# Kernel tuning notes

Hardware: AMD Instinct MI355X
Metric: run time of the kernel (lower is better)

## Reference

```python
import jax, jax.numpy as jnp
import numpy as np

NEG_SLOPE = 0.01  # torch F.leaky_relu default


def setup_inputs() -> dict:
    key = jax.random.key(0)
    k1, k2, k3, k4 = jax.random.split(key, 4)
    B, N, F_in, F_out = 16, 2048, 128, 128
    stdv = 1.0 / np.sqrt(F_out)
    h = jax.random.normal(k1, (B, N, F_in), dtype=jnp.float32)
    adj = jax.random.uniform(k2, (B, N, N), dtype=jnp.float32)
    W = jax.random.uniform(k3, (F_in, F_out), minval=-stdv, maxval=stdv, dtype=jnp.float32)
    a = jax.random.uniform(k4, (2 * F_out, 1), minval=-stdv, maxval=stdv, dtype=jnp.float32)
    return {"h": h, "adj": adj, "W": W, "a": a}


def reference(h, adj, W, a):
    # Wh: [B, N, F_out]
    Wh = jnp.matmul(h, W)
    F_out = W.shape[1]
    a1 = a[:F_out, 0]  # [F_out]
    a2 = a[F_out:, 0]  # [F_out]
    # concat-score factorizes: e[b,i,j] = leaky(Wh[b,i]@a1 + Wh[b,j]@a2)
    f1 = jnp.einsum('bnf,f->bn', Wh, a1)  # [B, N]
    f2 = jnp.einsum('bnf,f->bn', Wh, a2)  # [B, N]
    e = jax.nn.leaky_relu(f1[:, :, None] + f2[:, None, :], negative_slope=NEG_SLOPE)  # [B,N,N]
    # NOTE: original softmax is over dim=1 (row index i), faithfully preserved
    attention = jax.nn.softmax(e, axis=1)
    h_prime = jnp.einsum('bij,bjf->bif', attention, Wh)  # bmm
    return h_prime
```

## Files before the change

### kernel.cpp

```cpp
#include <hip/hip_runtime.h>

#define BB 16
#define NN 2048
#define FF 128
#define NEG 0.01f
#define CH 32
#define CL (NN / CH)

__global__ __launch_bounds__(256) void k_wh(const float* __restrict__ h,
                                            const float* __restrict__ Wg,
                                            const float* __restrict__ a,
                                            float* __restrict__ Wh,
                                            float* __restrict__ f1,
                                            float* __restrict__ f2) {
    __shared__ float Ws[64 * 128];
    __shared__ float hsT[64 * 36];

    const int tid  = threadIdx.x;
    const int fg   = tid & 31;
    const int slot = tid >> 5;
    const int f4   = fg * 4;
    const int rowBase = blockIdx.x * 32;

    float acc[4][4];
#pragma unroll
    for (int r = 0; r < 4; ++r)
#pragma unroll
        for (int c = 0; c < 4; ++c) acc[r][c] = 0.f;

    const float4* Wg4 = (const float4*)Wg;
    const float4* hg4 = (const float4*)h;

    for (int kh = 0; kh < 128; kh += 64) {
        __syncthreads();
        for (int idx = tid; idx < 64 * 32; idx += 256) {
            int kk = idx >> 5, ff = idx & 31;
            ((float4*)Ws)[kk * 32 + ff] = Wg4[(size_t)(kh + kk) * 32 + ff];
        }
#pragma unroll
        for (int pass = 0; pass < 2; ++pass) {
            int idx = pass * 256 + tid;
            int kq = idx & 15, row = idx >> 4;
            float4 h4 = hg4[(size_t)(rowBase + row) * 32 + (kh >> 2) + kq];
            hsT[(kq * 4 + 0) * 36 + row] = h4.x;
            hsT[(kq * 4 + 1) * 36 + row] = h4.y;
            hsT[(kq * 4 + 2) * 36 + row] = h4.z;
            hsT[(kq * 4 + 3) * 36 + row] = h4.w;
        }
        __syncthreads();
#pragma unroll 8
        for (int kk = 0; kk < 64; ++kk) {
            float4 wv = *(const float4*)&Ws[kk * 128 + f4];
            float4 hv = *(const float4*)&hsT[kk * 36 + slot * 4];
            acc[0][0] += hv.x * wv.x; acc[0][1] += hv.x * wv.y; acc[0][2] += hv.x * wv.z; acc[0][3] += hv.x * wv.w;
            acc[1][0] += hv.y * wv.x; acc[1][1] += hv.y * wv.y; acc[1][2] += hv.y * wv.z; acc[1][3] += hv.y * wv.w;
            acc[2][0] += hv.z * wv.x; acc[2][1] += hv.z * wv.y; acc[2][2] += hv.z * wv.z; acc[2][3] += hv.z * wv.w;
            acc[3][0] += hv.w * wv.x; acc[3][1] += hv.w * wv.y; acc[3][2] += hv.w * wv.z; acc[3][3] += hv.w * wv.w;
        }
    }

    const float4* ag4 = (const float4*)a;
    float4 a1v = ag4[fg];
    float4 a2v = ag4[32 + fg];

#pragma unroll
    for (int r = 0; r < 4; ++r) {
        int row = rowBase + slot * 4 + r;
        float4 o; o.x = acc[r][0]; o.y = acc[r][1]; o.z = acc[r][2]; o.w = acc[r][3];
        *(float4*)&Wh[(size_t)row * 128 + f4] = o;
        float p1 = acc[r][0] * a1v.x + acc[r][1] * a1v.y + acc[r][2] * a1v.z + acc[r][3] * a1v.w;
        float p2 = acc[r][0] * a2v.x + acc[r][1] * a2v.y + acc[r][2] * a2v.z + acc[r][3] * a2v.w;
#pragma unroll
        for (int m = 16; m >= 1; m >>= 1) {
            p1 += __shfl_xor(p1, m);
            p2 += __shfl_xor(p2, m);
        }
        if (fg == 0) { f1[row] = p1; f2[row] = p2; }
    }
}

__device__ __forceinline__ float wave_incl_scan(float s, int lane) {
#pragma unroll
    for (int m = 1; m <= 32; m <<= 1) {
        float o = __shfl_up(s, m);
        if (lane >= m) s += o;
    }
    return s;
}

#define WAVE_SYNC() do { __builtin_amdgcn_wave_barrier(); asm volatile("" ::: "memory"); } while (0)

__global__ __launch_bounds__(1024) void k_sort2(const float* __restrict__ f1,
                                                const float* __restrict__ f2,
                                                float* __restrict__ SF1g,
                                                float* __restrict__ PAg,
                                                float* __restrict__ SAg,
                                                float* __restrict__ SKg,
                                                int* __restrict__ PERM,
                                                int* __restrict__ KIDX) {
    __shared__ float sKey[NN];
    __shared__ int   sIdx[NN];
    __shared__ float wtot[16];

    const int tid  = threadIdx.x;
    const int lane = tid & 63;
    const int w    = tid >> 6;
    const int b    = blockIdx.x & 15;
    const int task = blockIdx.x >> 4;

    const float* f1b = f1 + b * NN;
    const float* f2b = f2 + b * NN;

    if (task == 0) {
        for (int i = tid; i < NN; i += 1024) sKey[i] = f1b[i];
    } else {
        for (int i = tid; i < NN; i += 1024) { sKey[i] = f2b[i]; sIdx[i] = i; }
    }

    int prevj = 1024;
    for (int k = 2; k <= NN; k <<= 1) {
        for (int j = k >> 1; j > 0; j >>= 1) {
            if (j >= 128 || prevj >= 128) __syncthreads();
            else WAVE_SYNC();
            int mask = j - 1;
            int i   = ((tid & ~mask) << 1) | (tid & mask);
            int ixj = i | j;
            bool up = ((i & k) == 0);
            float av = sKey[i], bv = sKey[ixj];
            if ((av > bv) == up) {
                sKey[i] = bv; sKey[ixj] = av;
                if (task == 1) { int t2 = sIdx[i]; sIdx[i] = sIdx[ixj]; sIdx[ixj] = t2; }
            }
            prevj = j;
        }
    }
    __syncthreads();

    if (task == 0) {
        for (int i = tid; i < NN; i += 1024) SF1g[b * NN + i] = sKey[i];
        const size_t pbase = (size_t)b * (NN + 1);
        {
            float a0 = expf(NEG * sKey[2 * tid]);
            float a1 = expf(NEG * sKey[2 * tid + 1]);
            float s = a0 + a1;
            float v = wave_incl_scan(s, lane);
            if (lane == 63) wtot[w] = v;
            __syncthreads();
            float off = 0.f;
#pragma unroll
            for (int ww = 0; ww < 16; ++ww) off += (ww < w) ? wtot[ww] : 0.f;
            float excl = off + v - s;
            PAg[pbase + 2 * tid]     = excl;
            PAg[pbase + 2 * tid + 1] = excl + a0;
            if (tid == 1023) PAg[pbase + NN] = off + v;
        }
        __syncthreads();
        {
            float y0 = expf(sKey[NN - 1 - 2 * tid]);
            float y1 = expf(sKey[NN - 2 - 2 * tid]);
            float s = y0 + y1;
            float v = wave_incl_scan(s, lane);
            if (lane == 63) wtot[w] = v;
            __syncthreads();
            float off = 0.f;
#pragma unroll
            for (int ww = 0; ww < 16; ++ww) off += (ww < w) ? wtot[ww] : 0.f;
            SAg[pbase + NN - 1 - 2 * tid] = off + (v - s) + y0;
            SAg[pbase + NN - 2 - 2 * tid] = off + v;
            if (tid == 0) SAg[pbase + NN] = 0.f;
        }
    } else {
        for (int i = tid; i < NN; i += 1024) {
            SKg[b * NN + i]  = sKey[i];
            PERM[b * NN + i] = sIdx[i];
        }
        for (int i = tid; i < NN; i += 1024) {
            float tau = -f1b[i];
            int lo = 0, hi = NN;
            while (lo < hi) { int m = (lo + hi) >> 1; if (sKey[m] <= tau) lo = m + 1; else hi = m; }
            KIDX[b * NN + i] = lo;
        }
    }
}

__global__ __launch_bounds__(256) void k_uw(const float* __restrict__ SF1g,
                                            const float* __restrict__ PAg,
                                            const float* __restrict__ SAg,
                                            const float* __restrict__ SKg,
                                            float* __restrict__ Uarr,
                                            float* __restrict__ Warr) {
    __shared__ float sS[NN];
    __shared__ float sP[NN + 1];
    __shared__ float sA[NN + 1];
    const int b = blockIdx.x, tid = threadIdx.x;
    const size_t pbase = (size_t)b * (NN + 1);
    for (int i = tid; i < NN; i += 256) sS[i] = SF1g[b * NN + i];
    for (int i = tid; i < NN + 1; i += 256) { sP[i] = PAg[pbase + i]; sA[i] = SAg[pbase + i]; }
    __syncthreads();
    for (int t = tid; t < NN; t += 256) {
        float f2v = SKg[b * NN + t];
        float tau = -f2v;
        int lo = 0, hi = NN;
        while (lo < hi) { int m = (lo + hi) >> 1; if (sS[m] <= tau) lo = m + 1; else hi = m; }
        float eS = expf(NEG * f2v);
        float eF = expf(f2v);
        float inv = 1.0f / (eS * sP[lo] + eF * sA[lo]);
        Uarr[b * NN + t] = eF * inv;
        Warr[b * NN + t] = eS * inv;
    }
}

__global__ __launch_bounds__(128) void k_chunk(const float* __restrict__ Wh,
                                               const float* __restrict__ Uarr,
                                               const float* __restrict__ Warr,
                                               const int* __restrict__ PERM,
                                               float* __restrict__ CU,
                                               float* __restrict__ CW) {
    int blk = blockIdx.x;
    int b = blk / CH, c = blk % CH;
    int f = threadIdx.x;
    int base = b * NN + c * CL;
    const float* Whb = Wh + (size_t)b * NN * FF;
    float aU = 0.f, aW = 0.f;
#pragma unroll 4
    for (int t = 0; t < CL; ++t) {
        int j = PERM[base + t];
        float uv = Uarr[base + t], wv = Warr[base + t];
        float whv = Whb[(size_t)j * FF + f];
        aU += uv * whv; aW += wv * whv;
    }
    CU[(size_t)blk * 128 + f] = aU;
    CW[(size_t)blk * 128 + f] = aW;
}

__global__ __launch_bounds__(128) void k_offsets(float* __restrict__ CU,
                                                 float* __restrict__ CW) {
    int b = blockIdx.x, f = threadIdx.x;
    float aU = 0.f, aW = 0.f;
#pragma unroll
    for (int c = 0; c < CH; ++c) {
        size_t idx = (size_t)(b * CH + c) * 128 + f;
        float tU = CU[idx], tW = CW[idx];
        CU[idx] = aU; CW[idx] = aW;
        aU += tU; aW += tW;
    }
}

__global__ __launch_bounds__(128) void k_prefix(const float* __restrict__ Wh,
                                                const float* __restrict__ Uarr,
                                                const float* __restrict__ Warr,
                                                const int* __restrict__ PERM,
                                                const float* __restrict__ CU,
                                                const float* __restrict__ CW,
                                                float* __restrict__ PU,
                                                float* __restrict__ PW) {
    int blk = blockIdx.x;
    int b = blk / CH, c = blk % CH;
    int f = threadIdx.x;
    int base = b * NN + c * CL;
    const float* Whb = Wh + (size_t)b * NN * FF;
    float aU = CU[(size_t)blk * 128 + f];
    float aW = CW[(size_t)blk * 128 + f];
    size_t rowB = (size_t)b * (NN + 1);
#pragma unroll 4
    for (int t = 0; t < CL; ++t) {
        int g = c * CL + t;
        PU[(rowB + g) * FF + f] = aU;
        PW[(rowB + g) * FF + f] = aW;
        int j = PERM[base + t];
        float whv = Whb[(size_t)j * FF + f];
        aU += Uarr[base + t] * whv;
        aW += Warr[base + t] * whv;
    }
    if (c == CH - 1) {
        PU[(rowB + NN) * FF + f] = aU;
        PW[(rowB + NN) * FF + f] = aW;
    }
}

__global__ __launch_bounds__(256) void k_out(const float* __restrict__ PU,
                                             const float* __restrict__ PW,
                                             const float* __restrict__ f1,
                                             const int* __restrict__ KIDX,
                                             float* __restrict__ out) {
    int rowId = blockIdx.x * 2 + (threadIdx.x >> 7);
    int f = threadIdx.x & 127;
    int b = rowId >> 11;
    int k = KIDX[rowId];
    float f1v = f1[rowId];
    float alpha = expf(NEG * f1v);
    float beta  = expf(f1v);
    size_t rowB = (size_t)b * (NN + 1);
    float totU = PU[(rowB + NN) * FF + f];
    float pu   = PU[(rowB + k) * FF + f];
    float pw   = PW[(rowB + k) * FF + f];
    out[(size_t)rowId * FF + f] = alpha * pw + beta * (totU - pu);
}

extern "C" void kernel_launch(void* const* d_in, const int* in_sizes, int n_in,
                              void* d_out, int out_size, void* d_ws, size_t ws_size,
                              hipStream_t stream) {
    const float* h  = (const float*)d_in[0];
    const float* W  = (const float*)d_in[2];
    const float* a  = (const float*)d_in[3];
    float* out = (float*)d_out;

    float* ws = (float*)d_ws;
    float* Wh   = ws;  ws += (size_t)BB * NN * FF;
    float* f1   = ws;  ws += BB * NN;
    float* f2   = ws;  ws += BB * NN;
    float* SF1  = ws;  ws += BB * NN;
    float* PA   = ws;  ws += BB * (NN + 1);
    float* SA   = ws;  ws += BB * (NN + 1);
    float* SK   = ws;  ws += BB * NN;
    float* Uarr = ws;  ws += BB * NN;
    float* Warr = ws;  ws += BB * NN;
    float* CU   = ws;  ws += BB * CH * FF;
    float* CW   = ws;  ws += BB * CH * FF;
    float* PU   = ws;  ws += (size_t)BB * (NN + 1) * FF;
    float* PW   = ws;  ws += (size_t)BB * (NN + 1) * FF;
    int* PERM = (int*)ws;  ws += BB * NN;
    int* KIDX = (int*)ws;

    k_wh     <<<(BB * NN) / 32, 256, 0, stream>>>(h, W, a, Wh, f1, f2);
    k_sort2  <<<2 * BB, 1024, 0, stream>>>(f1, f2, SF1, PA, SA, SK, PERM, KIDX);
    k_uw     <<<BB, 256, 0, stream>>>(SF1, PA, SA, SK, Uarr, Warr);
    k_chunk  <<<BB * CH, 128, 0, stream>>>(Wh, Uarr, Warr, PERM, CU, CW);
    k_offsets<<<BB, 128, 0, stream>>>(CU, CW);
    k_prefix <<<BB * CH, 128, 0, stream>>>(Wh, Uarr, Warr, PERM, CU, CW, PU, PW);
    k_out    <<<(BB * NN) / 2, 256, 0, stream>>>(PU, PW, f1, KIDX, out);
}
```

Before: 391.0 us.

## Fuse prefix and output stages, keeping per-chunk prefixes in shared memory

The global PU/PW prefix arrays, about 2×16×2049×128 floats written and then gathered, are removed. Each chunk block now rebuilds its local prefix rows in LDS and emits the output rows whose split index falls inside that chunk. The sort kernel buckets rows by chunk with a histogram, a scan and a scatter, and the offsets kernel is folded into the emit kernel as a redundant per-block sum over chunk totals. The chunk count rises from 32 to 128, which shortens each sequential chain but makes every block re-read all chunk totals and leaves output rows unevenly spread across blocks.

```diff
diff --git a/kernel.cpp b/kernel.cpp
--- a/kernel.cpp
+++ b/kernel.cpp
@@ -4,7 +4,7 @@
 #define NN 2048
 #define FF 128
 #define NEG 0.01f
-#define CH 32
+#define CH 128
 #define CL (NN / CH)
 
 __global__ __launch_bounds__(256) void k_wh(const float* __restrict__ h,
@@ -97,10 +97,15 @@
                                                 float* __restrict__ SAg,
                                                 float* __restrict__ SKg,
                                                 int* __restrict__ PERM,
-                                                int* __restrict__ KIDX) {
+                                                int* __restrict__ KIDX,
+                                                int* __restrict__ ROWS,
+                                                int* __restrict__ BOFF) {
     __shared__ float sKey[NN];
     __shared__ int   sIdx[NN];
     __shared__ float wtot[16];
+    __shared__ int   hist[CH];
+    __shared__ int   hscan[CH + 1];
+    __shared__ int   sbuf[CH];
 
     const int tid  = threadIdx.x;
     const int lane = tid & 63;
@@ -174,11 +179,38 @@
             SKg[b * NN + i]  = sKey[i];
             PERM[b * NN + i] = sIdx[i];
         }
+        if (tid < CH) hist[tid] = 0;
+        __syncthreads();
         for (int i = tid; i < NN; i += 1024) {
             float tau = -f1b[i];
             int lo = 0, hi = NN;
             while (lo < hi) { int m = (lo + hi) >> 1; if (sKey[m] <= tau) lo = m + 1; else hi = m; }
             KIDX[b * NN + i] = lo;
+            int c = lo / CL;
+            if (c > CH - 1) c = CH - 1;
+            sIdx[i] = c;
+            atomicAdd(&hist[c], 1);
+        }
+        __syncthreads();
+        if (tid < CH) sbuf[tid] = hist[tid];
+        for (int off = 1; off < CH; off <<= 1) {
+            __syncthreads();
+            int v = 0;
+            if (tid < CH) { v = sbuf[tid]; if (tid >= off) v += sbuf[tid - off]; }
+            __syncthreads();
+            if (tid < CH) sbuf[tid] = v;
+        }
+        __syncthreads();
+        if (tid == 0) hscan[0] = 0;
+        if (tid < CH) hscan[tid + 1] = sbuf[tid];
+        __syncthreads();
+        if (tid <= CH) BOFF[b * (CH + 1) + tid] = hscan[tid];
+        if (tid < CH) hist[tid] = hscan[tid];
+        __syncthreads();
+        for (int i = tid; i < NN; i += 1024) {
+            int c = sIdx[i];
+            int pos = atomicAdd(&hist[c], 1);
+            ROWS[b * NN + pos] = i;
         }
     }
 }
@@ -222,79 +254,68 @@
     int base = b * NN + c * CL;
     const float* Whb = Wh + (size_t)b * NN * FF;
     float aU = 0.f, aW = 0.f;
-#pragma unroll 4
+#pragma unroll
     for (int t = 0; t < CL; ++t) {
         int j = PERM[base + t];
         float uv = Uarr[base + t], wv = Warr[base + t];
         float whv = Whb[(size_t)j * FF + f];
         aU += uv * whv; aW += wv * whv;
     }
-    CU[(size_t)blk * 128 + f] = aU;
-    CW[(size_t)blk * 128 + f] = aW;
-}
-
-__global__ __launch_bounds__(128) void k_offsets(float* __restrict__ CU,
-                                                 float* __restrict__ CW) {
-    int b = blockIdx.x, f = threadIdx.x;
-    float aU = 0.f, aW = 0.f;
-#pragma unroll
-    for (int c = 0; c < CH; ++c) {
-        size_t idx = (size_t)(b * CH + c) * 128 + f;
-        float tU = CU[idx], tW = CW[idx];
-        CU[idx] = aU; CW[idx] = aW;
-        aU += tU; aW += tW;
-    }
-}
-
-__global__ __launch_bounds__(128) void k_prefix(const float* __restrict__ Wh,
-                                                const float* __restrict__ Uarr,
-                                                const float* __restrict__ Warr,
-                                                const int* __restrict__ PERM,
-                                                const float* __restrict__ CU,
-                                                const float* __restrict__ CW,
-                                                float* __restrict__ PU,
-                                                float* __restrict__ PW) {
-    int blk = blockIdx.x;
-    int b = blk / CH, c = blk % CH;
-    int f = threadIdx.x;
-    int base = b * NN + c * CL;
+    CU[(size_t)blk * FF + f] = aU;
+    CW[(size_t)blk * FF + f] = aW;
+}
+
+__global__ __launch_bounds__(128) void k_emit(const float* __restrict__ Wh,
+                                              const float* __restrict__ Uarr,
+                                              const float* __restrict__ Warr,
+                                              const int* __restrict__ PERM,
+                                              const float* __restrict__ CU,
+                                              const float* __restrict__ CW,
+                                              const float* __restrict__ f1,
+                                              const int* __restrict__ KIDX,
+                                              const int* __restrict__ ROWS,
+                                              const int* __restrict__ BOFF,
+                                              float* __restrict__ out) {
+    __shared__ float pU[CL + 1][FF];
+    __shared__ float pW[CL + 1][FF];
+
+    const int blk = blockIdx.x;
+    const int b = blk / CH, c = blk % CH;
+    const int f = threadIdx.x;
+
+    float aU = 0.f, aW = 0.f, totU = 0.f;
+#pragma unroll 4
+    for (int cc = 0; cc < CH; ++cc) {
+        float tU = CU[((size_t)b * CH + cc) * FF + f];
+        float tW = CW[((size_t)b * CH + cc) * FF + f];
+        if (cc < c) { aU += tU; aW += tW; }
+        totU += tU;
+    }
+
+    const int base = b * NN + c * CL;
     const float* Whb = Wh + (size_t)b * NN * FF;
-    float aU = CU[(size_t)blk * 128 + f];
-    float aW = CW[(size_t)blk * 128 + f];
-    size_t rowB = (size_t)b * (NN + 1);
-#pragma unroll 4
+#pragma unroll
     for (int t = 0; t < CL; ++t) {
-        int g = c * CL + t;
-        PU[(rowB + g) * FF + f] = aU;
-        PW[(rowB + g) * FF + f] = aW;
+        pU[t][f] = aU; pW[t][f] = aW;
         int j = PERM[base + t];
         float whv = Whb[(size_t)j * FF + f];
         aU += Uarr[base + t] * whv;
         aW += Warr[base + t] * whv;
     }
-    if (c == CH - 1) {
-        PU[(rowB + NN) * FF + f] = aU;
-        PW[(rowB + NN) * FF + f] = aW;
-    }
-}
-
-__global__ __launch_bounds__(256) void k_out(const float* __restrict__ PU,
-                                             const float* __restrict__ PW,
-                                             const float* __restrict__ f1,
-                                             const int* __restrict__ KIDX,
-                                             float* __restrict__ out) {
-    int rowId = blockIdx.x * 2 + (threadIdx.x >> 7);
-    int f = threadIdx.x & 127;
-    int b = rowId >> 11;
-    int k = KIDX[rowId];
-    float f1v = f1[rowId];
-    float alpha = expf(NEG * f1v);
-    float beta  = expf(f1v);
-    size_t rowB = (size_t)b * (NN + 1);
-    float totU = PU[(rowB + NN) * FF + f];
-    float pu   = PU[(rowB + k) * FF + f];
-    float pw   = PW[(rowB + k) * FF + f];
-    out[(size_t)rowId * FF + f] = alpha * pw + beta * (totU - pu);
+    pU[CL][f] = aU; pW[CL][f] = aW;
+    __syncthreads();
+
+    const int rb = BOFF[b * (CH + 1) + c];
+    const int re = BOFF[b * (CH + 1) + c + 1];
+    for (int idx = rb; idx < re; ++idx) {
+        int i = ROWS[b * NN + idx];
+        int k = KIDX[b * NN + i];
+        int r = k - c * CL;
+        float f1v = f1[b * NN + i];
+        float alpha = expf(NEG * f1v);
+        float beta  = expf(f1v);
+        out[((size_t)(b * NN + i)) * FF + f] = alpha * pW[r][f] + beta * (totU - pU[r][f]);
+    }
 }
 
 extern "C" void kernel_launch(void* const* d_in, const int* in_sizes, int n_in,
@@ -315,18 +336,16 @@
     float* SK   = ws;  ws += BB * NN;
     float* Uarr = ws;  ws += BB * NN;
     float* Warr = ws;  ws += BB * NN;
-    float* CU   = ws;  ws += BB * CH * FF;
-    float* CW   = ws;  ws += BB * CH * FF;
-    float* PU   = ws;  ws += (size_t)BB * (NN + 1) * FF;
-    float* PW   = ws;  ws += (size_t)BB * (NN + 1) * FF;
+    float* CU   = ws;  ws += (size_t)BB * CH * FF;
+    float* CW   = ws;  ws += (size_t)BB * CH * FF;
     int* PERM = (int*)ws;  ws += BB * NN;
-    int* KIDX = (int*)ws;
-
-    k_wh     <<<(BB * NN) / 32, 256, 0, stream>>>(h, W, a, Wh, f1, f2);
-    k_sort2  <<<2 * BB, 1024, 0, stream>>>(f1, f2, SF1, PA, SA, SK, PERM, KIDX);
-    k_uw     <<<BB, 256, 0, stream>>>(SF1, PA, SA, SK, Uarr, Warr);
-    k_chunk  <<<BB * CH, 128, 0, stream>>>(Wh, Uarr, Warr, PERM, CU, CW);
-    k_offsets<<<BB, 128, 0, stream>>>(CU, CW);
-    k_prefix <<<BB * CH, 128, 0, stream>>>(Wh, Uarr, Warr, PERM, CU, CW, PU, PW);
-    k_out    <<<(BB * NN) / 2, 256, 0, stream>>>(PU, PW, f1, KIDX, out);
-}
+    int* KIDX = (int*)ws;  ws += BB * NN;
+    int* ROWS = (int*)ws;  ws += BB * NN;
+    int* BOFF = (int*)ws;
+
+    k_wh    <<<(BB * NN) / 32, 256, 0, stream>>>(h, W, a, Wh, f1, f2);
+    k_sort2 <<<2 * BB, 1024, 0, stream>>>(f1, f2, SF1, PA, SA, SK, PERM, KIDX, ROWS, BOFF);
+    k_uw    <<<BB, 256, 0, stream>>>(SF1, PA, SA, SK, Uarr, Warr);
+    k_chunk <<<BB * CH, 128, 0, stream>>>(Wh, Uarr, Warr, PERM, CU, CW);
+    k_emit  <<<BB * CH, 128, 0, stream>>>(Wh, Uarr, Warr, PERM, CU, CW, f1, KIDX, ROWS, BOFF, out);
+}
```

Result: slower. 417.0 us (+6.6%).
